# Performance work log

Hardware: AMD Instinct MI355X
Metric: run time of the kernel (lower is better)

The kernel has to match this reference:

```python
import jax, jax.numpy as jnp
import numpy as np

EMB = 1024
HEAD = 64

def setup_inputs() -> dict:
    key = jax.random.key(0)
    k1, k2, k3, k4, k5 = jax.random.split(key, 5)
    x = jax.random.normal(k1, (4, 4096, EMB), dtype=jnp.float32)
    # qkv linear: weight [3*HEAD, EMB] torch-style -> store as [EMB, 3*HEAD]
    W_qkv = jax.random.normal(k2, (EMB, 3 * HEAD), dtype=jnp.float32) * (1.0 / np.sqrt(EMB))
    b_qkv = jax.random.normal(k3, (3 * HEAD,), dtype=jnp.float32) * 0.01
    W_out = jax.random.normal(k4, (HEAD, EMB), dtype=jnp.float32) * (1.0 / np.sqrt(HEAD))
    b_out = jax.random.normal(k5, (EMB,), dtype=jnp.float32) * 0.01
    return {"x": x, "W_qkv": W_qkv, "b_qkv": b_qkv, "W_out": W_out, "b_out": b_out}

def reference(x, W_qkv, b_qkv, W_out, b_out):
    qkv = jnp.einsum('bse,ed->bsd', x, W_qkv) + b_qkv            # [B,S,3H]
    q, k, v = jnp.split(qkv, 3, axis=-1)                          # each [B,S,H]
    scale = 1.0 / jnp.sqrt(jnp.asarray(q.shape[-1], q.dtype))
    scores = jnp.einsum('bqh,bkh->bqk', q, k) * scale             # [B,S,S]
    attn = jax.nn.softmax(scores, axis=-1)
    ctx = jnp.einsum('bqk,bkh->bqh', attn, v)                     # [B,S,H]
    return jnp.einsum('bqh,he->bqe', ctx, W_out) + b_out          # [B,S,E]
```

## Files before the change

### kernel.cpp

```cpp
#include <hip/hip_runtime.h>
#include <hip/hip_bf16.h>


#define LD 72

typedef __attribute__((ext_vector_type(8))) short short8;
typedef __attribute__((ext_vector_type(4))) short short4v;
typedef __attribute__((ext_vector_type(4))) float floatx4;

#define MFMA(a, b, c) __builtin_amdgcn_mfma_f32_16x16x32_bf16((a), (b), (c), 0, 0, 0)

__device__ __forceinline__ unsigned short f2bf(float f) {
  union { float f; unsigned u; } c; c.f = f;
  unsigned u = c.u + 0x7fffu + ((c.u >> 16) & 1u);
  return (unsigned short)(u >> 16);
}
__device__ __forceinline__ float asf(unsigned u) {
  union { unsigned u; float f; } c; c.u = u; return c.f;
}

__global__ __launch_bounds__(256) void prep_kernel(
    const float* __restrict__ Wqkv, const float* __restrict__ Wout,
    unsigned short* __restrict__ WtQkv, unsigned short* __restrict__ WtOut) {
  int idx = blockIdx.x * 256 + threadIdx.x;
  if (idx < 192 * 1024) {
    int n = idx >> 10, k = idx & 1023;
    WtQkv[idx] = f2bf(Wqkv[k * 192 + n]);
  } else if (idx < 192 * 1024 + 1024 * 64) {
    int j = idx - 192 * 1024;
    int e = j >> 6, d = j & 63;
    WtOut[j] = f2bf(Wout[d * 1024 + e]);
  }
}

__global__ __launch_bounds__(256, 1) void qkv_kernel(
    const float* __restrict__ x, const unsigned short* __restrict__ WtQkv,
    const float* __restrict__ bqkv,
    unsigned short* __restrict__ Qg, unsigned short* __restrict__ Kg,
    unsigned short* __restrict__ Vtg) {
  __shared__ __align__(16) unsigned short eQ[64 * LD];
  __shared__ __align__(16) unsigned short eK[64 * LD];
  __shared__ __align__(16) unsigned short eV[64 * LD];

  const int tid = threadIdx.x;
  const int wave = tid >> 6, lane = tid & 63, quad = lane >> 4, l16 = lane & 15;
  const int row0 = blockIdx.x * 64;
  const int rowbase = (wave & 1) * 32;
  const int colbase = (wave >> 1) * 96;

  floatx4 acc[2][6];
#pragma unroll
  for (int rt = 0; rt < 2; rt++)
#pragma unroll
    for (int t = 0; t < 6; t++) acc[rt][t] = (floatx4)(0.0f);

  const float* pA0 = x + (size_t)(row0 + rowbase + l16) * 1024 + quad * 8;
  const float* pA1 = pA0 + 16 * 1024;
  const unsigned short* pB[6];
#pragma unroll
  for (int t = 0; t < 6; t++)
    pB[t] = WtQkv + (size_t)(colbase + t * 16 + l16) * 1024 + quad * 8;

  float4 ax[2][2][2];
  uint4 bw[6][2];
#pragma unroll
  for (int kh = 0; kh < 2; kh++) {
    ax[0][kh][0] = *(const float4*)(pA0 + kh * 32);
    ax[0][kh][1] = *(const float4*)(pA0 + kh * 32 + 4);
    ax[1][kh][0] = *(const float4*)(pA1 + kh * 32);
    ax[1][kh][1] = *(const float4*)(pA1 + kh * 32 + 4);
  }
#pragma unroll
  for (int t = 0; t < 6; t++) {
    bw[t][0] = *(const uint4*)(pB[t]);
    bw[t][1] = *(const uint4*)(pB[t] + 32);
  }

  for (int kc = 0; kc < 16; kc++) {
    short8 af[2][2];
#pragma unroll
    for (int rt = 0; rt < 2; rt++)
#pragma unroll
      for (int kh = 0; kh < 2; kh++) {
        const float* f0 = (const float*)&ax[rt][kh][0];
        const float* f1 = (const float*)&ax[rt][kh][1];
        short8 a;
        a[0] = (short)f2bf(f0[0]); a[1] = (short)f2bf(f0[1]);
        a[2] = (short)f2bf(f0[2]); a[3] = (short)f2bf(f0[3]);
        a[4] = (short)f2bf(f1[0]); a[5] = (short)f2bf(f1[1]);
        a[6] = (short)f2bf(f1[2]); a[7] = (short)f2bf(f1[3]);
        af[rt][kh] = a;
      }
    if (kc < 15) {
#pragma unroll
      for (int kh = 0; kh < 2; kh++) {
        ax[0][kh][0] = *(const float4*)(pA0 + 64 + kh * 32);
        ax[0][kh][1] = *(const float4*)(pA0 + 64 + kh * 32 + 4);
        ax[1][kh][0] = *(const float4*)(pA1 + 64 + kh * 32);
        ax[1][kh][1] = *(const float4*)(pA1 + 64 + kh * 32 + 4);
      }
    }
#pragma unroll
    for (int t = 0; t < 6; t++) {
      short8 b0 = __builtin_bit_cast(short8, bw[t][0]);
      short8 b1 = __builtin_bit_cast(short8, bw[t][1]);
      if (kc < 15) {
        bw[t][0] = *(const uint4*)(pB[t] + 64);
        bw[t][1] = *(const uint4*)(pB[t] + 96);
      }
#pragma unroll
      for (int rt = 0; rt < 2; rt++) {
        acc[rt][t] = MFMA(af[rt][0], b0, acc[rt][t]);
        acc[rt][t] = MFMA(af[rt][1], b1, acc[rt][t]);
      }
    }
    pA0 += 64; pA1 += 64;
#pragma unroll
    for (int t = 0; t < 6; t++) pB[t] += 64;
  }

  const int b = row0 >> 12, srow = row0 & 4095;
#pragma unroll
  for (int rt = 0; rt < 2; rt++)
#pragma unroll
    for (int t = 0; t < 6; t++) {
      int tc = (wave >> 1) * 6 + t;
      int col = tc * 16 + l16;
      float bias = bqkv[col];
      int sec = col >> 6, d = col & 63;
#pragma unroll
      for (int r = 0; r < 4; r++) {
        int lrow = rowbase + rt * 16 + quad * 4 + r;
        float v = acc[rt][t][r] + bias;
        if (sec == 0)      eQ[lrow * LD + d] = f2bf(v * 0.125f);
        else if (sec == 1) eK[lrow * LD + d] = f2bf(v);
        else               eV[d * LD + lrow] = f2bf(v);
      }
    }
  __syncthreads();
#pragma unroll
  for (int i = 0; i < 2; i++) {
    int slot = tid + i * 256;
    int r = slot >> 3, sg = slot & 7;
    *(uint4*)(Qg + (size_t)(row0 + r) * 64 + sg * 8) = *(const uint4*)(&eQ[r * LD + sg * 8]);
    *(uint4*)(Kg + (size_t)(row0 + r) * 64 + sg * 8) = *(const uint4*)(&eK[r * LD + sg * 8]);
    int tile = slot >> 7, rem = slot & 127, d = rem >> 1, half = rem & 1;
    *(uint4*)(Vtg + (((size_t)b * 256 + (srow >> 4) + tile) * 64 + d) * 16 + half * 8)
        = *(const uint4*)(&eV[d * LD + tile * 16 + half * 8]);
  }
}

__global__ __launch_bounds__(256, 4) void attn_kernel(
    const unsigned short* __restrict__ Qg, const unsigned short* __restrict__ Kg,
    const unsigned short* __restrict__ Vtg,
    unsigned short* __restrict__ Opart, float* __restrict__ Lpart) {
  __shared__ __align__(16) unsigned short Ks[64 * LD];
  __shared__ __align__(16) unsigned short Vs[64 * LD];
  __shared__ __align__(16) unsigned short QP[64 * LD];

  const int tid = threadIdx.x;
  const int wave = tid >> 6, lane = tid & 63, quad = lane >> 4, l16 = lane & 15;
  const int bid = blockIdx.x;
  const int combo = bid & 15, qt = bid >> 4;
  const int b = combo >> 2, split = combo & 3;
  const int q0 = qt * 64, key0 = split * 1024;

  {
    int r = tid >> 2, seg = tid & 3;
    const uint4* s = (const uint4*)(Qg + ((size_t)b * 4096 + q0 + r) * 64 + seg * 16);
    *(uint4*)(&QP[r * LD + seg * 16])     = s[0];
    *(uint4*)(&QP[r * LD + seg * 16 + 8]) = s[1];
  }
  short8 aq0 = *(const short8*)(&QP[(wave * 16 + l16) * LD + quad * 8]);
  short8 aq1 = *(const short8*)(&QP[(wave * 16 + l16) * LD + 32 + quad * 8]);

  floatx4 o[4];
  float lsum[4];
#pragma unroll
  for (int t = 0; t < 4; t++) o[t] = (floatx4)(0.0f);
#pragma unroll
  for (int r = 0; r < 4; r++) lsum[r] = 0.0f;

  const int kr = tid >> 2, kseg = tid & 3;
  const unsigned short* Kbase = Kg + ((size_t)b * 4096 + key0) * 64;
  const unsigned short* Vt0 = Vtg + ((size_t)b * 256 + (key0 >> 4)) * 1024;

  uint4 pk0, pk1, pv0, pv1;
  pk0 = *(const uint4*)(Kbase + (size_t)kr * 64 + kseg * 16);
  pk1 = *(const uint4*)(Kbase + (size_t)kr * 64 + kseg * 16 + 8);
  pv0 = *(const uint4*)(Vt0 + ((size_t)kseg * 64 + kr) * 16);
  pv1 = *(const uint4*)(Vt0 + ((size_t)kseg * 64 + kr) * 16 + 8);

  unsigned short* Pw = &QP[wave * 16 * LD];

  for (int kc = 0; kc < 16; kc++) {
    __syncthreads();
    *(uint4*)(&Ks[kr * LD + kseg * 16])     = pk0;
    *(uint4*)(&Ks[kr * LD + kseg * 16 + 8]) = pk1;
    *(uint4*)(&Vs[kr * LD + kseg * 16])     = pv0;
    *(uint4*)(&Vs[kr * LD + kseg * 16 + 8]) = pv1;
    __syncthreads();
    if (kc < 15) {
      int nk = (kc + 1) * 64;
      int tl = (kc + 1) * 4 + kseg;
      pk0 = *(const uint4*)(Kbase + (size_t)(nk + kr) * 64 + kseg * 16);
      pk1 = *(const uint4*)(Kbase + (size_t)(nk + kr) * 64 + kseg * 16 + 8);
      pv0 = *(const uint4*)(Vt0 + ((size_t)tl * 64 + kr) * 16);
      pv1 = *(const uint4*)(Vt0 + ((size_t)tl * 64 + kr) * 16 + 8);
    }

    floatx4 sc[4];
#pragma unroll
    for (int t = 0; t < 4; t++) sc[t] = (floatx4)(0.0f);
#pragma unroll
    for (int t = 0; t < 4; t++) {
      short8 b0 = *(const short8*)(&Ks[(t * 16 + l16) * LD + quad * 8]);
      short8 b1 = *(const short8*)(&Ks[(t * 16 + l16) * LD + 32 + quad * 8]);
      sc[t] = MFMA(aq0, b0, sc[t]);
      sc[t] = MFMA(aq1, b1, sc[t]);
    }

#pragma unroll
    for (int r = 0; r < 4; r++) {
#pragma unroll
      for (int t = 0; t < 4; t++) {
        float pv = __expf(sc[t][r]);
        lsum[r] += pv;
        Pw[(quad * 4 + r) * LD + t * 16 + l16] = f2bf(pv);
      }
    }
    short8 ap0 = *(const short8*)(&Pw[l16 * LD + quad * 8]);
    short8 ap1 = *(const short8*)(&Pw[l16 * LD + 32 + quad * 8]);
#pragma unroll
    for (int t = 0; t < 4; t++) {
      short8 b0 = *(const short8*)(&Vs[(t * 16 + l16) * LD + quad * 8]);
      short8 b1 = *(const short8*)(&Vs[(t * 16 + l16) * LD + 32 + quad * 8]);
      o[t] = MFMA(ap0, b0, o[t]);
      o[t] = MFMA(ap1, b1, o[t]);
    }
  }

#pragma unroll
  for (int r = 0; r < 4; r++) {
#pragma unroll
    for (int off = 1; off < 16; off <<= 1) lsum[r] += __shfl_xor(lsum[r], off, 64);
  }

  unsigned short* Ob = Opart + ((size_t)bid * 64 + wave * 16) * 64;
#pragma unroll
  for (int t = 0; t < 4; t++)
#pragma unroll
    for (int r = 0; r < 4; r++)
      Ob[(quad * 4 + r) * 64 + t * 16 + l16] = f2bf(o[t][r]);
  if (l16 == 0) {
#pragma unroll
    for (int r = 0; r < 4; r++)
      Lpart[bid * 64 + wave * 16 + quad * 4 + r] = lsum[r];
  }
}

__global__ __launch_bounds__(256, 4) void combine_kernel(
    const unsigned short* __restrict__ Opart, const float* __restrict__ Lpart,
    const unsigned short* __restrict__ WtOut, const float* __restrict__ bout,
    float* __restrict__ out) {
  __shared__ __align__(16) unsigned short Cs[4][16 * LD];
  __shared__ __align__(16) unsigned short Wl[128 * LD];

  const int tid = threadIdx.x;
  const int wave = tid >> 6, lane = tid & 63, quad = lane >> 4, l16 = lane & 15;
  const int cid = blockIdx.x;
  const int eq = cid & 3, qt = (cid >> 2) & 63, b = cid >> 8;
  const int e0 = eq * 256;

  const int q = lane >> 2, d0 = (lane & 3) * 16;
  float accv[16];
#pragma unroll
  for (int i = 0; i < 16; i++) accv[i] = 0.0f;
  float lq = 0.0f;
#pragma unroll
  for (int s = 0; s < 4; s++) {
    int pid = qt * 16 + b * 4 + s;
    const unsigned short* src = Opart + ((size_t)pid * 64 + wave * 16 + q) * 64 + d0;
    uint4 h0 = *(const uint4*)src;
    uint4 h1 = *(const uint4*)(src + 8);
    const unsigned* hw = (const unsigned*)&h0;
#pragma unroll
    for (int i = 0; i < 4; i++) {
      accv[2 * i]     += asf(hw[i] << 16);
      accv[2 * i + 1] += asf(hw[i] & 0xFFFF0000u);
    }
    const unsigned* hw1 = (const unsigned*)&h1;
#pragma unroll
    for (int i = 0; i < 4; i++) {
      accv[8 + 2 * i]     += asf(hw1[i] << 16);
      accv[8 + 2 * i + 1] += asf(hw1[i] & 0xFFFF0000u);
    }
    lq += Lpart[pid * 64 + wave * 16 + q];
  }
  float inv = 1.0f / lq;
  short8 c0, c1;
#pragma unroll
  for (int i = 0; i < 8; i++) {
    c0[i] = (short)f2bf(accv[i] * inv);
    c1[i] = (short)f2bf(accv[8 + i] * inv);
  }
  *(short8*)(&Cs[wave][q * LD + d0])     = c0;
  *(short8*)(&Cs[wave][q * LD + d0 + 8]) = c1;
  short8 ao0 = *(const short8*)(&Cs[wave][l16 * LD + quad * 8]);
  short8 ao1 = *(const short8*)(&Cs[wave][l16 * LD + 32 + quad * 8]);

  const size_t orow0 = (size_t)b * 4096 + qt * 64 + wave * 16;
#pragma unroll 1
  for (int ec = 0; ec < 2; ec++) {
    int ebase = e0 + ec * 128;
    __syncthreads();
    {
      int er = tid >> 1, half = tid & 1;
      const uint4* s = (const uint4*)(WtOut + (size_t)(ebase + er) * 64 + half * 32);
      uint4 w0 = s[0], w1 = s[1], w2 = s[2], w3 = s[3];
      *(uint4*)(&Wl[er * LD + half * 32])      = w0;
      *(uint4*)(&Wl[er * LD + half * 32 + 8])  = w1;
      *(uint4*)(&Wl[er * LD + half * 32 + 16]) = w2;
      *(uint4*)(&Wl[er * LD + half * 32 + 24]) = w3;
    }
    __syncthreads();
    floatx4 a2[8];
#pragma unroll
    for (int t = 0; t < 8; t++) a2[t] = (floatx4)(0.0f);
#pragma unroll
    for (int t = 0; t < 8; t++) {
      short8 b0 = *(const short8*)(&Wl[(t * 16 + l16) * LD + quad * 8]);
      short8 b1 = *(const short8*)(&Wl[(t * 16 + l16) * LD + 32 + quad * 8]);
      a2[t] = MFMA(ao0, b0, a2[t]);
      a2[t] = MFMA(ao1, b1, a2[t]);
    }
#pragma unroll
    for (int t = 0; t < 8; t++) {
      int e = ebase + t * 16 + l16;
      float bo = bout[e];
#pragma unroll
      for (int r = 0; r < 4; r++)
        out[(orow0 + quad * 4 + r) * 1024 + e] = a2[t][r] + bo;
    }
  }
}

extern "C" void kernel_launch(void* const* d_in, const int* in_sizes, int n_in,
                              void* d_out, int out_size, void* d_ws, size_t ws_size,
                              hipStream_t stream) {
  const float* x    = (const float*)d_in[0];
  const float* Wqkv = (const float*)d_in[1];
  const float* bqkv = (const float*)d_in[2];
  const float* Wout = (const float*)d_in[3];
  const float* bout = (const float*)d_in[4];
  float* out = (float*)d_out;

  unsigned short* ws = (unsigned short*)d_ws;
  unsigned short* Qg    = ws;
  unsigned short* Kg    = Qg + 1048576;
  unsigned short* Vtg   = Kg + 1048576;
  unsigned short* WtQkv = Vtg + 1048576;
  unsigned short* WtOut = WtQkv + 196608;
  unsigned short* Opart = WtOut + 65536;
  float*          Lpart = (float*)(Opart + 4194304);

  prep_kernel<<<1024, 256, 0, stream>>>(Wqkv, Wout, WtQkv, WtOut);
  qkv_kernel<<<256, 256, 0, stream>>>(x, WtQkv, bqkv, Qg, Kg, Vtg);
  attn_kernel<<<1024, 256, 0, stream>>>(Qg, Kg, Vtg, Opart, Lpart);
  combine_kernel<<<1024, 256, 0, stream>>>(Opart, Lpart, WtOut, bout, out);
}
```

Before: 198.3 us.

## Shrink QKV projection tile to 16 rows for four-times more blocks

The QKV projection kernel now gives each block 16 rows instead of 64, and each wave computes a 16x48 slice of the output. This launches 1024 blocks instead of 256 and raises launch bounds to 4 blocks per CU, so the 256-CU GPU gets more than one block per CU and more memory-level parallelism. The cost is that each block reuses the weight tile across fewer rows, so the weights are read from cache four times as often, and each wave issues fewer MFMAs per load.

```diff
diff --git a/kernel.cpp b/kernel.cpp
--- a/kernel.cpp
+++ b/kernel.cpp
@@ -33,120 +33,102 @@
   }
 }
 
-__global__ __launch_bounds__(256, 1) void qkv_kernel(
+__global__ __launch_bounds__(256, 4) void qkv_kernel(
     const float* __restrict__ x, const unsigned short* __restrict__ WtQkv,
     const float* __restrict__ bqkv,
     unsigned short* __restrict__ Qg, unsigned short* __restrict__ Kg,
     unsigned short* __restrict__ Vtg) {
-  __shared__ __align__(16) unsigned short eQ[64 * LD];
-  __shared__ __align__(16) unsigned short eK[64 * LD];
-  __shared__ __align__(16) unsigned short eV[64 * LD];
+  __shared__ __align__(16) unsigned short eQ[16 * LD];
+  __shared__ __align__(16) unsigned short eK[16 * LD];
+  __shared__ __align__(16) unsigned short eV[64 * 24];
 
   const int tid = threadIdx.x;
   const int wave = tid >> 6, lane = tid & 63, quad = lane >> 4, l16 = lane & 15;
-  const int row0 = blockIdx.x * 64;
-  const int rowbase = (wave & 1) * 32;
-  const int colbase = (wave >> 1) * 96;
-
-  floatx4 acc[2][6];
-#pragma unroll
-  for (int rt = 0; rt < 2; rt++)
-#pragma unroll
-    for (int t = 0; t < 6; t++) acc[rt][t] = (floatx4)(0.0f);
-
-  const float* pA0 = x + (size_t)(row0 + rowbase + l16) * 1024 + quad * 8;
-  const float* pA1 = pA0 + 16 * 1024;
-  const unsigned short* pB[6];
-#pragma unroll
-  for (int t = 0; t < 6; t++)
+  const int row0 = blockIdx.x * 16;
+  const int colbase = wave * 48;
+
+  floatx4 acc[3];
+#pragma unroll
+  for (int t = 0; t < 3; t++) acc[t] = (floatx4)(0.0f);
+
+  const float* pA = x + (size_t)(row0 + l16) * 1024 + quad * 8;
+  const unsigned short* pB[3];
+#pragma unroll
+  for (int t = 0; t < 3; t++)
     pB[t] = WtQkv + (size_t)(colbase + t * 16 + l16) * 1024 + quad * 8;
 
-  float4 ax[2][2][2];
-  uint4 bw[6][2];
+  float4 ax[2][2];
+  uint4 bw[3][2];
 #pragma unroll
   for (int kh = 0; kh < 2; kh++) {
-    ax[0][kh][0] = *(const float4*)(pA0 + kh * 32);
-    ax[0][kh][1] = *(const float4*)(pA0 + kh * 32 + 4);
-    ax[1][kh][0] = *(const float4*)(pA1 + kh * 32);
-    ax[1][kh][1] = *(const float4*)(pA1 + kh * 32 + 4);
-  }
-#pragma unroll
-  for (int t = 0; t < 6; t++) {
+    ax[kh][0] = *(const float4*)(pA + kh * 32);
+    ax[kh][1] = *(const float4*)(pA + kh * 32 + 4);
+  }
+#pragma unroll
+  for (int t = 0; t < 3; t++) {
     bw[t][0] = *(const uint4*)(pB[t]);
     bw[t][1] = *(const uint4*)(pB[t] + 32);
   }
 
   for (int kc = 0; kc < 16; kc++) {
-    short8 af[2][2];
-#pragma unroll
-    for (int rt = 0; rt < 2; rt++)
+    short8 af[2];
+#pragma unroll
+    for (int kh = 0; kh < 2; kh++) {
+      const float* f0 = (const float*)&ax[kh][0];
+      const float* f1 = (const float*)&ax[kh][1];
+      short8 a;
+      a[0] = (short)f2bf(f0[0]); a[1] = (short)f2bf(f0[1]);
+      a[2] = (short)f2bf(f0[2]); a[3] = (short)f2bf(f0[3]);
+      a[4] = (short)f2bf(f1[0]); a[5] = (short)f2bf(f1[1]);
+      a[6] = (short)f2bf(f1[2]); a[7] = (short)f2bf(f1[3]);
+      af[kh] = a;
+    }
+    if (kc < 15) {
 #pragma unroll
       for (int kh = 0; kh < 2; kh++) {
-        const float* f0 = (const float*)&ax[rt][kh][0];
-        const float* f1 = (const float*)&ax[rt][kh][1];
-        short8 a;
-        a[0] = (short)f2bf(f0[0]); a[1] = (short)f2bf(f0[1]);
-        a[2] = (short)f2bf(f0[2]); a[3] = (short)f2bf(f0[3]);
-        a[4] = (short)f2bf(f1[0]); a[5] = (short)f2bf(f1[1]);
-        a[6] = (short)f2bf(f1[2]); a[7] = (short)f2bf(f1[3]);
-        af[rt][kh] = a;
+        ax[kh][0] = *(const float4*)(pA + 64 + kh * 32);
+        ax[kh][1] = *(const float4*)(pA + 64 + kh * 32 + 4);
       }
-    if (kc < 15) {
-#pragma unroll
-      for (int kh = 0; kh < 2; kh++) {
-        ax[0][kh][0] = *(const float4*)(pA0 + 64 + kh * 32);
-        ax[0][kh][1] = *(const float4*)(pA0 + 64 + kh * 32 + 4);
-        ax[1][kh][0] = *(const float4*)(pA1 + 64 + kh * 32);
-        ax[1][kh][1] = *(const float4*)(pA1 + 64 + kh * 32 + 4);
-      }
-    }
-#pragma unroll
-    for (int t = 0; t < 6; t++) {
+    }
+#pragma unroll
+    for (int t = 0; t < 3; t++) {
       short8 b0 = __builtin_bit_cast(short8, bw[t][0]);
       short8 b1 = __builtin_bit_cast(short8, bw[t][1]);
       if (kc < 15) {
         bw[t][0] = *(const uint4*)(pB[t] + 64);
         bw[t][1] = *(const uint4*)(pB[t] + 96);
       }
-#pragma unroll
-      for (int rt = 0; rt < 2; rt++) {
-        acc[rt][t] = MFMA(af[rt][0], b0, acc[rt][t]);
-        acc[rt][t] = MFMA(af[rt][1], b1, acc[rt][t]);
-      }
-    }
-    pA0 += 64; pA1 += 64;
-#pragma unroll
-    for (int t = 0; t < 6; t++) pB[t] += 64;
+      acc[t] = MFMA(af[0], b0, acc[t]);
+      acc[t] = MFMA(af[1], b1, acc[t]);
+    }
+    pA += 64;
+#pragma unroll
+    for (int t = 0; t < 3; t++) pB[t] += 64;
   }
 
   const int b = row0 >> 12, srow = row0 & 4095;
 #pragma unroll
-  for (int rt = 0; rt < 2; rt++)
-#pragma unroll
-    for (int t = 0; t < 6; t++) {
-      int tc = (wave >> 1) * 6 + t;
-      int col = tc * 16 + l16;
-      float bias = bqkv[col];
-      int sec = col >> 6, d = col & 63;
-#pragma unroll
-      for (int r = 0; r < 4; r++) {
-        int lrow = rowbase + rt * 16 + quad * 4 + r;
-        float v = acc[rt][t][r] + bias;
-        if (sec == 0)      eQ[lrow * LD + d] = f2bf(v * 0.125f);
-        else if (sec == 1) eK[lrow * LD + d] = f2bf(v);
-        else               eV[d * LD + lrow] = f2bf(v);
-      }
-    }
+  for (int t = 0; t < 3; t++) {
+    int col = colbase + t * 16 + l16;
+    float bias = bqkv[col];
+    int sec = col >> 6, d = col & 63;
+#pragma unroll
+    for (int r = 0; r < 4; r++) {
+      int lrow = quad * 4 + r;
+      float v = acc[t][r] + bias;
+      if (sec == 0)      eQ[lrow * LD + d] = f2bf(v * 0.125f);
+      else if (sec == 1) eK[lrow * LD + d] = f2bf(v);
+      else               eV[d * 24 + lrow] = f2bf(v);
+    }
+  }
   __syncthreads();
-#pragma unroll
-  for (int i = 0; i < 2; i++) {
-    int slot = tid + i * 256;
-    int r = slot >> 3, sg = slot & 7;
-    *(uint4*)(Qg + (size_t)(row0 + r) * 64 + sg * 8) = *(const uint4*)(&eQ[r * LD + sg * 8]);
-    *(uint4*)(Kg + (size_t)(row0 + r) * 64 + sg * 8) = *(const uint4*)(&eK[r * LD + sg * 8]);
-    int tile = slot >> 7, rem = slot & 127, d = rem >> 1, half = rem & 1;
-    *(uint4*)(Vtg + (((size_t)b * 256 + (srow >> 4) + tile) * 64 + d) * 16 + half * 8)
-        = *(const uint4*)(&eV[d * LD + tile * 16 + half * 8]);
+  {
+    int r = tid >> 4, sg = tid & 15;
+    *(uint2*)(Qg + (size_t)(row0 + r) * 64 + sg * 4) = *(const uint2*)(&eQ[r * LD + sg * 4]);
+    *(uint2*)(Kg + (size_t)(row0 + r) * 64 + sg * 4) = *(const uint2*)(&eK[r * LD + sg * 4]);
+    int d = tid >> 2, s2 = tid & 3;
+    *(uint2*)(Vtg + (((size_t)b * 256 + (srow >> 4)) * 64 + d) * 16 + s2 * 4)
+        = *(const uint2*)(&eV[d * 24 + s2 * 4]);
   }
 }
 
@@ -365,7 +347,7 @@
   float*          Lpart = (float*)(Opart + 4194304);
 
   prep_kernel<<<1024, 256, 0, stream>>>(Wqkv, Wout, WtQkv, WtOut);
-  qkv_kernel<<<256, 256, 0, stream>>>(x, WtQkv, bqkv, Qg, Kg, Vtg);
+  qkv_kernel<<<1024, 256, 0, stream>>>(x, WtQkv, bqkv, Qg, Kg, Vtg);
   attn_kernel<<<1024, 256, 0, stream>>>(Qg, Kg, Vtg, Opart, Lpart);
   combine_kernel<<<1024, 256, 0, stream>>>(Opart, Lpart, WtOut, bout, out);
 }
```

Result: slower. 231.7 us (+16.8%).
